# Kernel optimization log

Measured on AMD Instinct MI355X. Metric: run time of the kernel, lower is better.

The kernel has to match this reference:

```python
import jax, jax.numpy as jnp
import numpy as np

ALPHA = 0.2  # LeakyReLU slope
NEG = -1e9


def setup_inputs() -> dict:
    key = jax.random.key(0)
    k1, k2, k3, k4, k5 = jax.random.split(key, 5)
    B, N, F_IN, F_OUT, H = 8, 1024, 512, 256, 8
    x = jax.random.normal(k1, (B, N, F_IN), dtype=jnp.float32)
    adj = jax.random.randint(k2, (B, N, N), 0, 2, dtype=jnp.int32)
    W = jax.random.normal(k3, (H, F_OUT, F_IN), dtype=jnp.float32) * 0.05
    a1 = jax.random.normal(k4, (H, F_OUT), dtype=jnp.float32) * 0.05
    a2 = jax.random.normal(k5, (H, F_OUT), dtype=jnp.float32) * 0.05
    return {"x": x, "adj": adj, "W": W, "a1": a1, "a2": a2}


def _head(x, adj_zero, W, a1, a2):
    # x: (B,N,F_in), W: (F_out,F_in), a1/a2: (F_out,)
    h = jnp.einsum('bnf,of->bno', x, W)              # (B,N,F_out)
    f1 = jnp.einsum('bno,o->bn', h, a1)              # (B,N)
    f2 = jnp.einsum('bno,o->bn', h, a2)              # (B,N)
    e = f1[:, :, None] + f2[:, None, :]              # (B,N,N) broadcast add
    e = jax.nn.leaky_relu(e, negative_slope=ALPHA)
    e = jnp.where(adj_zero, NEG, e)                  # adjacency mask
    att = jax.nn.softmax(e, axis=2)
    return jnp.einsum('bnm,bmo->bno', att, h)        # (B,N,F_out)


def reference(x, adj, W, a1, a2):
    adj_zero = (adj == 0)
    # vmap over heads; sum of elu(head outputs)
    heads = jax.vmap(lambda w, u, v: _head(x, adj_zero, w, u, v))(W, a1, a2)  # (H,B,N,F_out)
    out = jnp.sum(jax.nn.elu(heads), axis=0)         # (B,N,F_out)
    return jax.nn.log_softmax(out, axis=2)
```

## Files before the change

### kernel.cpp

```cpp
#include <hip/hip_runtime.h>
#include <math.h>

#define B_    8
#define N_    1024
#define FIN   512
#define FOUT  256
#define H_    8
#define ALPHA 0.2f

#define XT (B_ * N_ * FIN)
#define WT (H_ * FOUT * FIN)

typedef short s16x8 __attribute__((ext_vector_type(8)));
typedef float f32x4 __attribute__((ext_vector_type(4)));

__device__ __forceinline__ unsigned short f2bf(float f) {
  unsigned int u = __float_as_uint(f);
  u = (u + 0x7FFFu + ((u >> 16) & 1u)) >> 16;
  return (unsigned short)u;
}

__device__ __forceinline__ unsigned int pk4_fp8(float a, float b, float c,
                                                float d) {
  int u = __builtin_amdgcn_cvt_pk_fp8_f32(a, b, 0, false);
  u = __builtin_amdgcn_cvt_pk_fp8_f32(c, d, u, true);
  return (unsigned int)u;
}

#if __has_builtin(__builtin_amdgcn_cvt_pk_f32_fp8)
#define HAVE_DEQ4 1
__device__ __forceinline__ float deq4(unsigned int u) {
  const auto a = __builtin_amdgcn_cvt_pk_f32_fp8((int)u, false);
  const auto b = __builtin_amdgcn_cvt_pk_f32_fp8((int)u, true);
  return (a[0] + a[1]) + (b[0] + b[1]);
}
#else
#define HAVE_DEQ4 0
__device__ __forceinline__ float q8e4m3(float p) {
  if (p >= 0.015625f) {
    unsigned int u = __float_as_uint(p);
    u = (u + 0x7FFFFu + ((u >> 20) & 1u)) & 0xFFF00000u;
    return __uint_as_float(u);
  }
  return (p + 16384.f) - 16384.f;
}
#endif

__device__ __forceinline__ void gload16(const void* g, void* l) {
  __builtin_amdgcn_global_load_lds(
      (const __attribute__((address_space(1))) unsigned int*)g,
      (__attribute__((address_space(3))) unsigned int*)l, 16, 0, 0);
}


#define CVB  ((XT + WT) / 1024)
#define ZRB  192
#define PKB  ((B_ * N_ * 32) / 256)

__global__ __launch_bounds__(256) void prep(
    const float* __restrict__ x, const float* __restrict__ W,
    const int* __restrict__ adj, unsigned short* __restrict__ xb,
    unsigned short* __restrict__ Wb, float* __restrict__ f12,
    unsigned int* __restrict__ adjP) {
  const int blk = blockIdx.x;
  if (blk >= CVB + ZRB) {
    const int dw = (blk - CVB - ZRB) * 256 + threadIdx.x;
    const int r = dw >> 5, pd = dw & 31;
    const int q = pd >> 3, c8 = pd & 7;
    const int* ap = adj + (size_t)r * N_;
    unsigned int out = 0;
#pragma unroll
    for (int i = 0; i < 4; ++i) {
      const int jb = (c8 * 4 + i) * 32 + q * 8;
      int4 v0 = *(const int4*)(ap + jb);
      int4 v1 = *(const int4*)(ap + jb + 4);
      unsigned int byte = 0;
      byte |= (v0.x ? 1u : 0u) << 0; byte |= (v0.y ? 1u : 0u) << 1;
      byte |= (v0.z ? 1u : 0u) << 2; byte |= (v0.w ? 1u : 0u) << 3;
      byte |= (v1.x ? 1u : 0u) << 4; byte |= (v1.y ? 1u : 0u) << 5;
      byte |= (v1.z ? 1u : 0u) << 6; byte |= (v1.w ? 1u : 0u) << 7;
      out |= byte << (i * 8);
    }
    adjP[dw] = out;
    return;
  }
  if (blk >= CVB) {
    const int i = (blk - CVB) * 256 + threadIdx.x;
    ((float4*)f12)[i] = make_float4(0.f, 0.f, 0.f, 0.f);
    return;
  }
  const int i = (blk * 256 + threadIdx.x) * 4;
  const float* src;
  unsigned short* dst;
  int off;
  if (i < XT) { src = x; dst = xb; off = i; }
  else        { src = W; dst = Wb; off = i - XT; }
  float4 v = *(const float4*)(src + off);
  ushort4 s;
  s.x = f2bf(v.x); s.y = f2bf(v.y); s.z = f2bf(v.z); s.w = f2bf(v.w);
  *(ushort4*)(dst + off) = s;
}

__global__ __launch_bounds__(256, 3) void proj_mfma(
    const unsigned short* __restrict__ xb, const unsigned short* __restrict__ Wb,
    const float* __restrict__ a1, const float* __restrict__ a2,
    unsigned char* __restrict__ htq, float* __restrict__ f1,
    float* __restrict__ f2) {
  __shared__ __align__(16) unsigned short As[128 * 64];
  __shared__ __align__(16) unsigned short Bs[128 * 64];
  const int gid = blockIdx.x;
  const int b = gid & 7;
  const int mt_ = (gid >> 3) & 7;
  const int ot_ = (gid >> 6) & 1;
  const int h = gid >> 7;
  const int hb = h * B_ + b;
  const int m0 = mt_ * 128, o0 = ot_ * 128;
  const int t = threadIdx.x, w = t >> 6, lane = t & 63;
  const int col = lane & 15, quad = lane >> 4;

  const int srow = t >> 3;
  const int sseg = (t & 7) ^ (srow & 7);
  const unsigned short* agp = xb + (size_t)(b * N_ + m0 + srow) * FIN + sseg * 8;
  const unsigned short* bgp = Wb + (size_t)(h * FOUT + o0 + srow) * FIN + sseg * 8;

  f32x4 acc[2][8];
  const f32x4 z4 = {0.f, 0.f, 0.f, 0.f};
#pragma unroll
  for (int mt = 0; mt < 2; ++mt)
#pragma unroll
    for (int ot = 0; ot < 8; ++ot) acc[mt][ot] = z4;

  for (int it = 0; it < FIN / 64; ++it) {
    __syncthreads();
    const int k0 = it * 64;
#pragma unroll
    for (int i2 = 0; i2 < 4; ++i2) {
      gload16(agp + (size_t)i2 * 32 * FIN + k0, &As[i2 * 2048 + t * 8]);
      gload16(bgp + (size_t)i2 * 32 * FIN + k0, &Bs[i2 * 2048 + t * 8]);
    }
    __syncthreads();

#pragma unroll
    for (int kb = 0; kb < 2; ++kb) {
      s16x8 af[2], bf[8];
#pragma unroll
      for (int mt = 0; mt < 2; ++mt) {
        const int row = w * 32 + mt * 16 + col;
        af[mt] = *(const s16x8*)&As[row * 64 + ((kb * 4 + quad) ^ (row & 7)) * 8];
      }
#pragma unroll
      for (int ot = 0; ot < 8; ++ot) {
        const int row = ot * 16 + col;
        bf[ot] = *(const s16x8*)&Bs[row * 64 + ((kb * 4 + quad) ^ (row & 7)) * 8];
      }
#pragma unroll
      for (int mt = 0; mt < 2; ++mt)
#pragma unroll
        for (int ot = 0; ot < 8; ++ot)
          acc[mt][ot] = __builtin_amdgcn_mfma_f32_16x16x32_bf16(af[mt], bf[ot],
                                                                acc[mt][ot], 0, 0, 0);
    }
  }

  const int kkw = (m0 >> 5) + w;
  float pf1[2][4] = {{0.f}}, pf2[2][4] = {{0.f}};
#pragma unroll
  for (int mt = 0; mt < 2; ++mt) {
#pragma unroll
    for (int ot = 0; ot < 8; ++ot) {
      const int o = o0 + ot * 16 + col;
      const float va1 = a1[h * FOUT + o], va2 = a2[h * FOUT + o];
      const int otg = (o0 >> 4) + ot;
      unsigned char* fb =
          htq + (((size_t)(hb * 16 + otg) * 32 + kkw) << 9);
      const unsigned int q =
          pk4_fp8(acc[mt][ot][0], acc[mt][ot][1], acc[mt][ot][2], acc[mt][ot][3]);
      *(unsigned int*)(fb + (2 * mt + (quad >> 1)) * 128 + col * 8 +
                       (quad & 1) * 4) = q;
#pragma unroll
      for (int r = 0; r < 4; ++r) {
        pf1[mt][r] += acc[mt][ot][r] * va1;
        pf2[mt][r] += acc[mt][ot][r] * va2;
      }
    }
  }
#pragma unroll
  for (int off = 1; off <= 8; off <<= 1)
#pragma unroll
    for (int mt = 0; mt < 2; ++mt)
#pragma unroll
      for (int r = 0; r < 4; ++r) {
        pf1[mt][r] += __shfl_xor(pf1[mt][r], off);
        pf2[mt][r] += __shfl_xor(pf2[mt][r], off);
      }
  if (col == 0) {
#pragma unroll
    for (int mt = 0; mt < 2; ++mt)
#pragma unroll
      for (int r = 0; r < 4; ++r) {
        const int n = m0 + w * 32 + mt * 16 + quad * 4 + r;
        atomicAdd(&f1[hb * N_ + n], pf1[mt][r]);
        atomicAdd(&f2[hb * N_ + n], pf2[mt][r]);
      }
  }
}

__global__ __launch_bounds__(256) void wgen(
    const float* __restrict__ f1, const float* __restrict__ f2,
    const unsigned int* __restrict__ adjP, unsigned char* __restrict__ wq,
    float* __restrict__ dnm) {
  const int id = blockIdx.x;
  const int b = id & 7, h = (id >> 3) & 7;
  const int rbg = (id >> 6) & 15;
  const int kkh = id >> 10;
  const int w = threadIdx.x >> 6, lane = threadIdx.x & 63;
  const int col = lane & 15, quad = lane >> 4;
  const int hb = h * B_ + b;
  const int rb = rbg * 4 + w;
  const int row = rb * 16 + col;

  const float* f2r = f2 + (size_t)hb * N_;
  float m2 = -3.0e38f;
#pragma unroll
  for (int c = 0; c < 16; ++c) m2 = fmaxf(m2, f2r[lane + c * 64]);
#pragma unroll
  for (int off = 32; off; off >>= 1) m2 = fmaxf(m2, __shfl_xor(m2, off));

  const float f1i = f1[(size_t)hb * N_ + row];
  const float tb = f1i + m2;
  const float mhat = fmaxf(tb, ALPHA * tb);

  const unsigned int* adp = adjP + ((size_t)(b * N_ + row) << 5) + quad * 8;
  const float* f2p = f2r + quad * 8;
  unsigned char* wp = wq + (((size_t)(hb * 64 + rb) * 32) << 9) + lane * 8;

  float dsum = 0.f;
#pragma unroll
  for (int k4i = 0; k4i < 4; ++k4i) {
    const int k4 = kkh * 4 + k4i;
    const unsigned int ad = adp[k4];
#pragma unroll
    for (int k2 = 0; k2 < 4; ++k2) {
      const int kk = k4 * 4 + k2;
      const unsigned int ab = (ad >> (k2 * 8)) & 0xFFu;
      const float4 fA = *(const float4*)(f2p + kk * 32);
      const float4 fB = *(const float4*)(f2p + kk * 32 + 4);
      float ex[8];
#pragma unroll
      for (int j = 0; j < 8; ++j) {
        const float fv = j < 4 ? ((const float*)&fA)[j]
                               : ((const float*)&fB)[j - 4];
        const float tt = f1i + fv;
        const float l = fmaxf(tt, ALPHA * tt);
        const float p = __expf(l - mhat);
        ex[j] = ((ab >> j) & 1u) ? p : 0.f;
      }
      const unsigned int lo = pk4_fp8(ex[0], ex[1], ex[2], ex[3]);
      const unsigned int hi = pk4_fp8(ex[4], ex[5], ex[6], ex[7]);
#if HAVE_DEQ4
      dsum += deq4(lo) + deq4(hi);
#else
#pragma unroll
      for (int j = 0; j < 8; ++j) dsum += q8e4m3(ex[j]);
#endif
      *(uint2*)(wp + kk * 512) = make_uint2(lo, hi);
    }
  }
  dsum += __shfl_xor(dsum, 16);
  dsum += __shfl_xor(dsum, 32);
  if (quad == 0) atomicAdd(&dnm[(size_t)hb * N_ + row], dsum);
}

__global__ __launch_bounds__(256, 4) void pv(
    const unsigned char* __restrict__ htq, const unsigned char* __restrict__ wq,
    const float* __restrict__ dnm, float* __restrict__ p0,
    float* __restrict__ p1, float* __restrict__ p2, float* __restrict__ p3) {
  __shared__ __align__(16) unsigned char Bsh[2][16384];
  const int id = blockIdx.x;
  const int b = id & 7;
  const int g0 = (id >> 3) & 3;
  const int oq = (id >> 5) & 3;
  const int it = id >> 7;
  const int tid = threadIdx.x;
  const int w = tid >> 6, lane = tid & 63;
  const int col = lane & 15, quad = lane >> 4;
  const int rb = it * 8 + w * 2;

  const int hb0 = (g0 * 2 + 0) * B_ + b;
  const int hb1 = (g0 * 2 + 1) * B_ + b;
  const unsigned char* ap0 =
      wq + (((size_t)(hb0 * 64 + rb) * 32) << 9) + lane * 8;
  const unsigned char* ap1 =
      wq + (((size_t)(hb1 * 64 + rb) * 32) << 9) + lane * 8;
  const unsigned char* bp0 = htq + (((size_t)(hb0 * 16 + oq * 4) * 32) << 9);
  const unsigned char* bp1 = htq + (((size_t)(hb1 * 16 + oq * 4) * 32) << 9);

  float hsum[2][4][4];
#pragma unroll
  for (int g = 0; g < 2; ++g)
#pragma unroll
    for (int t = 0; t < 4; ++t)
#pragma unroll
      for (int r = 0; r < 4; ++r) hsum[g][t][r] = 0.f;

  f32x4 acc[2][4];
  const f32x4 z4 = {0.f, 0.f, 0.f, 0.f};
  float4 den0, den1;

#define STAGE(buf, bptr, c)                                                  \
  do {                                                                       \
    _Pragma("unroll")                                                        \
    for (int t = 0; t < 4; ++t)                                              \
      gload16(bptr + t * 16384 + (c) * 4096 + tid * 16,                      \
              &Bsh[buf][t * 4096 + tid * 16]);                               \
  } while (0)

  STAGE(0, bp0, 0);
  __syncthreads();

#pragma unroll
  for (int cc = 0; cc < 8; ++cc) {
    const int hh = cc >> 2;
    const int c = cc & 3;
    const int cur = cc & 1;
    const unsigned char* ap = hh ? ap1 : ap0;

    if (cc < 7) {
      const unsigned char* nbp = ((cc + 1) >> 2) ? bp1 : bp0;
      STAGE(1 - cur, nbp, (cc + 1) & 3);
    }

    if (c == 0) {
      const float* dr = dnm + (size_t)(hh ? hb1 : hb0) * N_ + quad * 4;
      den0 = *(const float4*)(dr + (rb + 0) * 16);
      den1 = *(const float4*)(dr + (rb + 1) * 16);
#pragma unroll
      for (int g = 0; g < 2; ++g)
#pragma unroll
        for (int t = 0; t < 4; ++t) acc[g][t] = z4;
    }

    long A0[8], A1[8];
#pragma unroll
    for (int kkl = 0; kkl < 8; ++kkl) {
      A0[kkl] = *(const long*)(ap + (size_t)(c * 8 + kkl) * 512);
      A1[kkl] = *(const long*)(ap + 16384 + (size_t)(c * 8 + kkl) * 512);
    }

    const unsigned char* bl = &Bsh[cur][lane * 8];
#pragma unroll
    for (int kkl = 0; kkl < 8; ++kkl) {
      const long b0 = *(const long*)(bl + 0 * 4096 + kkl * 512);
      const long b1 = *(const long*)(bl + 1 * 4096 + kkl * 512);
      const long b2 = *(const long*)(bl + 2 * 4096 + kkl * 512);
      const long b3 = *(const long*)(bl + 3 * 4096 + kkl * 512);
      __builtin_amdgcn_s_setprio(1);
      acc[0][0] = __builtin_amdgcn_mfma_f32_16x16x32_fp8_fp8(A0[kkl], b0, acc[0][0], 0, 0, 0);
      acc[1][0] = __builtin_amdgcn_mfma_f32_16x16x32_fp8_fp8(A1[kkl], b0, acc[1][0], 0, 0, 0);
      acc[0][1] = __builtin_amdgcn_mfma_f32_16x16x32_fp8_fp8(A0[kkl], b1, acc[0][1], 0, 0, 0);
      acc[1][1] = __builtin_amdgcn_mfma_f32_16x16x32_fp8_fp8(A1[kkl], b1, acc[1][1], 0, 0, 0);
      acc[0][2] = __builtin_amdgcn_mfma_f32_16x16x32_fp8_fp8(A0[kkl], b2, acc[0][2], 0, 0, 0);
      acc[1][2] = __builtin_amdgcn_mfma_f32_16x16x32_fp8_fp8(A1[kkl], b2, acc[1][2], 0, 0, 0);
      acc[0][3] = __builtin_amdgcn_mfma_f32_16x16x32_fp8_fp8(A0[kkl], b3, acc[0][3], 0, 0, 0);
      acc[1][3] = __builtin_amdgcn_mfma_f32_16x16x32_fp8_fp8(A1[kkl], b3, acc[1][3], 0, 0, 0);
      __builtin_amdgcn_s_setprio(0);
    }

    if (c == 3) {
#pragma unroll
      for (int g = 0; g < 2; ++g)
#pragma unroll
        for (int r = 0; r < 4; ++r) {
          const float dv = (g == 0) ? (&den0.x)[r] : (&den1.x)[r];
          const float inv = 1.0f / dv;
#pragma unroll
          for (int t = 0; t < 4; ++t) {
            const float oh = acc[g][t][r] * inv;
            hsum[g][t][r] += oh > 0.f ? oh : __expf(oh) - 1.f;
          }
        }
    }

    if (cc < 7) __syncthreads();
  }
#undef STAGE

  float* pdst = (g0 == 0) ? p0 : (g0 == 1) ? p1 : (g0 == 2) ? p2 : p3;
#pragma unroll
  for (int g = 0; g < 2; ++g)
#pragma unroll
    for (int t = 0; t < 4; ++t)
#pragma unroll
      for (int r = 0; r < 4; ++r) {
        const int orow = (rb + g) * 16 + quad * 4 + r;
        pdst[(size_t)(b * N_ + orow) * FOUT + oq * 64 + t * 16 + col] =
            hsum[g][t][r];
      }
}

__global__ __launch_bounds__(256) void logsm(
    const float* __restrict__ p0, const float* __restrict__ p1,
    const float* __restrict__ p2, const float* __restrict__ p3,
    float* __restrict__ out) {
  const int row = blockIdx.x * 4 + (threadIdx.x >> 6);
  const int lane = threadIdx.x & 63;
  const size_t base = (size_t)row * FOUT;
  float v[4];
  float m = -3.0e38f;
#pragma unroll
  for (int c = 0; c < 4; ++c) {
    const size_t idx = base + c * 64 + lane;
    v[c] = p0[idx] + p1[idx] + p2[idx] + p3[idx];
    m = fmaxf(m, v[c]);
  }
#pragma unroll
  for (int off = 32; off; off >>= 1) m = fmaxf(m, __shfl_xor(m, off));
  float s = 0.f;
#pragma unroll
  for (int c = 0; c < 4; ++c) s += __expf(v[c] - m);
#pragma unroll
  for (int off = 32; off; off >>= 1) s += __shfl_xor(s, off);
  const float lg = m + logf(s);
#pragma unroll
  for (int c = 0; c < 4; ++c)
    out[base + c * 64 + lane] = v[c] - lg;
}

extern "C" void kernel_launch(void* const* d_in, const int* in_sizes, int n_in,
                              void* d_out, int out_size, void* d_ws,
                              size_t ws_size, hipStream_t stream) {
  const float* x   = (const float*)d_in[0];
  const int*   adj = (const int*)d_in[1];
  const float* W   = (const float*)d_in[2];
  const float* a1  = (const float*)d_in[3];
  const float* a2  = (const float*)d_in[4];
  float* out = (float*)d_out;

  unsigned char* htq = (unsigned char*)d_ws;
  unsigned short* xb = (unsigned short*)(htq + (size_t)H_ * B_ * FOUT * N_);
  unsigned short* Wb = xb + (size_t)XT;
  float* f1 = (float*)(Wb + (size_t)WT);
  float* f2 = f1 + (size_t)H_ * B_ * N_;
  float* dnm = f2 + (size_t)H_ * B_ * N_;
  float* part2 = dnm + (size_t)H_ * B_ * N_;
  float* part3 = part2 + (size_t)B_ * N_ * FOUT;
  unsigned int* adjP = (unsigned int*)(part3 + (size_t)B_ * N_ * FOUT);
  unsigned char* wq = (unsigned char*)(adjP + (size_t)B_ * N_ * 32);
  float* part1 = (float*)xb;

  prep<<<CVB + ZRB + PKB, 256, 0, stream>>>(x, W, adj, xb, Wb, f1, adjP);

  proj_mfma<<<1024, 256, 0, stream>>>(xb, Wb, a1, a2, htq, f1, f2);

  wgen<<<2048, 256, 0, stream>>>(f1, f2, adjP, wq, dnm);

  pv<<<1024, 256, 0, stream>>>(htq, wq, dnm, out, part1, part2, part3);

  logsm<<<(B_ * N_) / 4, 256, 0, stream>>>(out, part1, part2, part3, out);
}
```

Before: 194.6 us.

## Pipeline pv kernel with half-size LDS stages and register-prefetched A operands

Restructures the pv kernel's main loop into 16 smaller phases with half-size double-buffered LDS tiles. The A operands for the next phase are prefetched into ping-pong registers while the current MFMAs run. Barriers now use explicit vmcnt waits instead of __syncthreads, so global loads stay in flight across phases. The launch-bounds occupancy hint is dropped, which gives up the occupancy guarantee in exchange for more registers. The gain is meant to come from hiding global-load latency behind MFMA work, at the cost of more barriers and relying on a hand-tuned vmcnt count.

```diff
diff --git a/kernel.cpp b/kernel.cpp
--- a/kernel.cpp
+++ b/kernel.cpp
@@ -271,11 +271,11 @@
   if (quad == 0) atomicAdd(&dnm[(size_t)hb * N_ + row], dsum);
 }
 
-__global__ __launch_bounds__(256, 4) void pv(
+__global__ __launch_bounds__(256) void pv(
     const unsigned char* __restrict__ htq, const unsigned char* __restrict__ wq,
     const float* __restrict__ dnm, float* __restrict__ p0,
     float* __restrict__ p1, float* __restrict__ p2, float* __restrict__ p3) {
-  __shared__ __align__(16) unsigned char Bsh[2][16384];
+  __shared__ __align__(16) unsigned char Bsh[2][8192];
   const int id = blockIdx.x;
   const int b = id & 7;
   const int g0 = (id >> 3) & 3;
@@ -295,6 +295,10 @@
   const unsigned char* bp0 = htq + (((size_t)(hb0 * 16 + oq * 4) * 32) << 9);
   const unsigned char* bp1 = htq + (((size_t)(hb1 * 16 + oq * 4) * 32) << 9);
 
+  const int flat0 = tid * 16, flat1 = 4096 + tid * 16;
+  const int gs0 = (flat0 >> 11) * 16384 + (flat0 & 2047);
+  const int gs1 = (flat1 >> 11) * 16384 + (flat1 & 2047);
+
   float hsum[2][4][4];
 #pragma unroll
   for (int g = 0; g < 2; ++g)
@@ -306,84 +310,92 @@
   f32x4 acc[2][4];
   const f32x4 z4 = {0.f, 0.f, 0.f, 0.f};
   float4 den0, den1;
-
-#define STAGE(buf, bptr, c)                                                  \
-  do {                                                                       \
-    _Pragma("unroll")                                                        \
-    for (int t = 0; t < 4; ++t)                                              \
-      gload16(bptr + t * 16384 + (c) * 4096 + tid * 16,                      \
-              &Bsh[buf][t * 4096 + tid * 16]);                               \
-  } while (0)
-
-  STAGE(0, bp0, 0);
-  __syncthreads();
-
-#pragma unroll
-  for (int cc = 0; cc < 8; ++cc) {
-    const int hh = cc >> 2;
-    const int c = cc & 3;
-    const int cur = cc & 1;
-    const unsigned char* ap = hh ? ap1 : ap0;
-
-    if (cc < 7) {
-      const unsigned char* nbp = ((cc + 1) >> 2) ? bp1 : bp0;
-      STAGE(1 - cur, nbp, (cc + 1) & 3);
-    }
-
-    if (c == 0) {
-      const float* dr = dnm + (size_t)(hh ? hb1 : hb0) * N_ + quad * 4;
-      den0 = *(const float4*)(dr + (rb + 0) * 16);
-      den1 = *(const float4*)(dr + (rb + 1) * 16);
-#pragma unroll
-      for (int g = 0; g < 2; ++g)
-#pragma unroll
-        for (int t = 0; t < 4; ++t) acc[g][t] = z4;
-    }
-
-    long A0[8], A1[8];
-#pragma unroll
-    for (int kkl = 0; kkl < 8; ++kkl) {
-      A0[kkl] = *(const long*)(ap + (size_t)(c * 8 + kkl) * 512);
-      A1[kkl] = *(const long*)(ap + 16384 + (size_t)(c * 8 + kkl) * 512);
-    }
-
-    const unsigned char* bl = &Bsh[cur][lane * 8];
-#pragma unroll
-    for (int kkl = 0; kkl < 8; ++kkl) {
-      const long b0 = *(const long*)(bl + 0 * 4096 + kkl * 512);
-      const long b1 = *(const long*)(bl + 1 * 4096 + kkl * 512);
-      const long b2 = *(const long*)(bl + 2 * 4096 + kkl * 512);
-      const long b3 = *(const long*)(bl + 3 * 4096 + kkl * 512);
-      __builtin_amdgcn_s_setprio(1);
-      acc[0][0] = __builtin_amdgcn_mfma_f32_16x16x32_fp8_fp8(A0[kkl], b0, acc[0][0], 0, 0, 0);
-      acc[1][0] = __builtin_amdgcn_mfma_f32_16x16x32_fp8_fp8(A1[kkl], b0, acc[1][0], 0, 0, 0);
-      acc[0][1] = __builtin_amdgcn_mfma_f32_16x16x32_fp8_fp8(A0[kkl], b1, acc[0][1], 0, 0, 0);
-      acc[1][1] = __builtin_amdgcn_mfma_f32_16x16x32_fp8_fp8(A1[kkl], b1, acc[1][1], 0, 0, 0);
-      acc[0][2] = __builtin_amdgcn_mfma_f32_16x16x32_fp8_fp8(A0[kkl], b2, acc[0][2], 0, 0, 0);
-      acc[1][2] = __builtin_amdgcn_mfma_f32_16x16x32_fp8_fp8(A1[kkl], b2, acc[1][2], 0, 0, 0);
-      acc[0][3] = __builtin_amdgcn_mfma_f32_16x16x32_fp8_fp8(A0[kkl], b3, acc[0][3], 0, 0, 0);
-      acc[1][3] = __builtin_amdgcn_mfma_f32_16x16x32_fp8_fp8(A1[kkl], b3, acc[1][3], 0, 0, 0);
-      __builtin_amdgcn_s_setprio(0);
-    }
-
-    if (c == 3) {
-#pragma unroll
-      for (int g = 0; g < 2; ++g)
-#pragma unroll
-        for (int r = 0; r < 4; ++r) {
-          const float dv = (g == 0) ? (&den0.x)[r] : (&den1.x)[r];
-          const float inv = 1.0f / dv;
-#pragma unroll
-          for (int t = 0; t < 4; ++t) {
-            const float oh = acc[g][t][r] * inv;
-            hsum[g][t][r] += oh > 0.f ? oh : __expf(oh) - 1.f;
-          }
-        }
-    }
-
-    if (cc < 7) __syncthreads();
-  }
-#undef STAGE
+  long Ae[8], Ao[8];
+
+  {
+    const float* dr = dnm + (size_t)hb0 * N_ + quad * 4;
+    den0 = *(const float4*)(dr + (rb + 0) * 16);
+    den1 = *(const float4*)(dr + (rb + 1) * 16);
+  }
+  gload16(bp0 + gs0, &Bsh[0][flat0]);
+  gload16(bp0 + gs1, &Bsh[0][flat1]);
+#pragma unroll
+  for (int k = 0; k < 4; ++k) {
+    Ae[k] = *(const long*)(ap0 + k * 512);
+    Ae[4 + k] = *(const long*)(ap0 + 16384 + k * 512);
+  }
+  asm volatile("s_waitcnt vmcnt(8)" ::: "memory");
+  __builtin_amdgcn_s_barrier();
+
+#define PHASE(cc, Acur, Anxt)                                                \
+  {                                                                          \
+    const int c_ = (cc) & 7;                                                 \
+    const int cur_ = (cc) & 1;                                               \
+    if ((cc) == 8) {        \
+      const float* dr_ = dnm + (size_t)hb1 * N_ + quad * 4;                  \
+      den0 = *(const float4*)(dr_ + (rb + 0) * 16);                          \
+      den1 = *(const float4*)(dr_ + (rb + 1) * 16);                          \
+    }                                                                        \
+    if ((cc) < 15) {                                                         \
+      const int cn_ = (cc) + 1;                                              \
+      const unsigned char* gb_ = (cn_ >= 8) ? bp1 : bp0;                     \
+      const int co_ = (cn_ & 7) * 2048;                                      \
+      gload16(gb_ + gs0 + co_, &Bsh[1 - cur_][flat0]);                       \
+      gload16(gb_ + gs1 + co_, &Bsh[1 - cur_][flat1]);                       \
+      const unsigned char* an_ = (cn_ >= 8) ? ap1 : ap0;                     \
+      const int ko_ = (cn_ & 7) * 2048;                                      \
+      _Pragma("unroll")                                                      \
+      for (int k = 0; k < 4; ++k) {                                          \
+        Anxt[k] = *(const long*)(an_ + ko_ + k * 512);                       \
+        Anxt[4 + k] = *(const long*)(an_ + 16384 + ko_ + k * 512);           \
+      }                                                                      \
+    }                                                                        \
+    if (c_ == 0) {                                                           \
+      _Pragma("unroll") for (int g = 0; g < 2; ++g)                          \
+      _Pragma("unroll") for (int t = 0; t < 4; ++t) acc[g][t] = z4;          \
+    }                                                                        \
+    {                                                                        \
+      const unsigned char* bl_ = &Bsh[cur_][lane * 8];                       \
+      _Pragma("unroll")                                                      \
+      for (int kkl = 0; kkl < 4; ++kkl) {                                    \
+        const long b0_ = *(const long*)(bl_ + 0 * 2048 + kkl * 512);         \
+        const long b1_ = *(const long*)(bl_ + 1 * 2048 + kkl * 512);         \
+        const long b2_ = *(const long*)(bl_ + 2 * 2048 + kkl * 512);         \
+        const long b3_ = *(const long*)(bl_ + 3 * 2048 + kkl * 512);         \
+        __builtin_amdgcn_s_setprio(1);                                       \
+        acc[0][0] = __builtin_amdgcn_mfma_f32_16x16x32_fp8_fp8(Acur[kkl], b0_, acc[0][0], 0, 0, 0); \
+        acc[1][0] = __builtin_amdgcn_mfma_f32_16x16x32_fp8_fp8(Acur[4 + kkl], b0_, acc[1][0], 0, 0, 0); \
+        acc[0][1] = __builtin_amdgcn_mfma_f32_16x16x32_fp8_fp8(Acur[kkl], b1_, acc[0][1], 0, 0, 0); \
+        acc[1][1] = __builtin_amdgcn_mfma_f32_16x16x32_fp8_fp8(Acur[4 + kkl], b1_, acc[1][1], 0, 0, 0); \
+        acc[0][2] = __builtin_amdgcn_mfma_f32_16x16x32_fp8_fp8(Acur[kkl], b2_, acc[0][2], 0, 0, 0); \
+        acc[1][2] = __builtin_amdgcn_mfma_f32_16x16x32_fp8_fp8(Acur[4 + kkl], b2_, acc[1][2], 0, 0, 0); \
+        acc[0][3] = __builtin_amdgcn_mfma_f32_16x16x32_fp8_fp8(Acur[kkl], b3_, acc[0][3], 0, 0, 0); \
+        acc[1][3] = __builtin_amdgcn_mfma_f32_16x16x32_fp8_fp8(Acur[4 + kkl], b3_, acc[1][3], 0, 0, 0); \
+        __builtin_amdgcn_s_setprio(0);                                       \
+      }                                                                      \
+    }                                                                        \
+    if (c_ == 7) {                \
+      _Pragma("unroll") for (int g = 0; g < 2; ++g)                          \
+      _Pragma("unroll") for (int r = 0; r < 4; ++r) {                        \
+        const float dv_ = (g == 0) ? (&den0.x)[r] : (&den1.x)[r];            \
+        const float inv_ = 1.0f / dv_;                                       \
+        _Pragma("unroll") for (int t = 0; t < 4; ++t) {                      \
+          const float oh_ = acc[g][t][r] * inv_;                             \
+          hsum[g][t][r] += oh_ > 0.f ? oh_ : __expf(oh_) - 1.f;              \
+        }                                                                    \
+      }                                                                      \
+    }                                                                        \
+    if ((cc) < 15) {                                                         \
+      asm volatile("s_waitcnt vmcnt(8)" ::: "memory");       \
+      __builtin_amdgcn_s_barrier();                        \
+    }                                                                        \
+  }
+
+  PHASE(0, Ae, Ao)  PHASE(1, Ao, Ae)  PHASE(2, Ae, Ao)  PHASE(3, Ao, Ae)
+  PHASE(4, Ae, Ao)  PHASE(5, Ao, Ae)  PHASE(6, Ae, Ao)  PHASE(7, Ao, Ae)
+  PHASE(8, Ae, Ao)  PHASE(9, Ao, Ae)  PHASE(10, Ae, Ao) PHASE(11, Ao, Ae)
+  PHASE(12, Ae, Ao) PHASE(13, Ao, Ae) PHASE(14, Ae, Ao) PHASE(15, Ao, Ae)
+#undef PHASE
 
   float* pdst = (g0 == 0) ? p0 : (g0 == 1) ? p1 : (g0 == 2) ? p2 : p3;
 #pragma unroll
```

Result: no change. 191.5 us (median of 2 runs) (-1.6%).

## Fuse attention weight generation into PV kernel, drop wgen and fp8 weight buffer

Applied to the files above, without the earlier changes.

Removes the separate wgen kernel, which wrote fp8 attention weights and denominators to global memory. The pv kernel now computes the exp-weights on the fly from f1, f2 staged in shared memory and the packed adjacency, feeding them straight into the fp8 MFMAs. Work is re-split so each block handles one head and half of the output columns. Per-head ELU outputs go to 8 partial buffers that logsm sums. This avoids a global round trip of the weight tensor and one launch, but recomputes the exps for each output-column half and doubles partial-output traffic. ZRB also drops from 192 to 128 since dnm no longer needs zeroing.

```diff
diff --git a/kernel.cpp b/kernel.cpp
--- a/kernel.cpp
+++ b/kernel.cpp
@@ -52,9 +52,32 @@
       (__attribute__((address_space(3))) unsigned int*)l, 16, 0, 0);
 }
 
+__device__ __forceinline__ long gen8(unsigned int ab, const float4 fA,
+                                     const float4 fB, float f1i, float mhat,
+                                     float& dsum) {
+  float ex[8];
+#pragma unroll
+  for (int j = 0; j < 8; ++j) {
+    const float fv = j < 4 ? ((const float*)&fA)[j] : ((const float*)&fB)[j - 4];
+    const float tt = f1i + fv;
+    const float l = fmaxf(tt, ALPHA * tt);
+    const float p = __expf(l - mhat);
+    ex[j] = ((ab >> j) & 1u) ? p : 0.f;
+  }
+  const unsigned int lo = pk4_fp8(ex[0], ex[1], ex[2], ex[3]);
+  const unsigned int hi = pk4_fp8(ex[4], ex[5], ex[6], ex[7]);
+#if HAVE_DEQ4
+  dsum += deq4(lo) + deq4(hi);
+#else
+#pragma unroll
+  for (int j = 0; j < 8; ++j) dsum += q8e4m3(ex[j]);
+#endif
+  return (long)(((unsigned long long)hi << 32) | (unsigned long long)lo);
+}
+
 
 #define CVB  ((XT + WT) / 1024)
-#define ZRB  192
+#define ZRB  128
 #define PKB  ((B_ * N_ * 32) / 256)
 
 __global__ __launch_bounds__(256) void prep(
@@ -205,212 +228,145 @@
   }
 }
 
-__global__ __launch_bounds__(256) void wgen(
-    const float* __restrict__ f1, const float* __restrict__ f2,
-    const unsigned int* __restrict__ adjP, unsigned char* __restrict__ wq,
-    float* __restrict__ dnm) {
-  const int id = blockIdx.x;
-  const int b = id & 7, h = (id >> 3) & 7;
-  const int rbg = (id >> 6) & 15;
-  const int kkh = id >> 10;
-  const int w = threadIdx.x >> 6, lane = threadIdx.x & 63;
-  const int col = lane & 15, quad = lane >> 4;
-  const int hb = h * B_ + b;
-  const int rb = rbg * 4 + w;
-  const int row = rb * 16 + col;
-
-  const float* f2r = f2 + (size_t)hb * N_;
-  float m2 = -3.0e38f;
-#pragma unroll
-  for (int c = 0; c < 16; ++c) m2 = fmaxf(m2, f2r[lane + c * 64]);
-#pragma unroll
-  for (int off = 32; off; off >>= 1) m2 = fmaxf(m2, __shfl_xor(m2, off));
-
-  const float f1i = f1[(size_t)hb * N_ + row];
-  const float tb = f1i + m2;
-  const float mhat = fmaxf(tb, ALPHA * tb);
-
-  const unsigned int* adp = adjP + ((size_t)(b * N_ + row) << 5) + quad * 8;
-  const float* f2p = f2r + quad * 8;
-  unsigned char* wp = wq + (((size_t)(hb * 64 + rb) * 32) << 9) + lane * 8;
-
-  float dsum = 0.f;
-#pragma unroll
-  for (int k4i = 0; k4i < 4; ++k4i) {
-    const int k4 = kkh * 4 + k4i;
-    const unsigned int ad = adp[k4];
-#pragma unroll
-    for (int k2 = 0; k2 < 4; ++k2) {
-      const int kk = k4 * 4 + k2;
-      const unsigned int ab = (ad >> (k2 * 8)) & 0xFFu;
-      const float4 fA = *(const float4*)(f2p + kk * 32);
-      const float4 fB = *(const float4*)(f2p + kk * 32 + 4);
-      float ex[8];
-#pragma unroll
-      for (int j = 0; j < 8; ++j) {
-        const float fv = j < 4 ? ((const float*)&fA)[j]
-                               : ((const float*)&fB)[j - 4];
-        const float tt = f1i + fv;
-        const float l = fmaxf(tt, ALPHA * tt);
-        const float p = __expf(l - mhat);
-        ex[j] = ((ab >> j) & 1u) ? p : 0.f;
-      }
-      const unsigned int lo = pk4_fp8(ex[0], ex[1], ex[2], ex[3]);
-      const unsigned int hi = pk4_fp8(ex[4], ex[5], ex[6], ex[7]);
-#if HAVE_DEQ4
-      dsum += deq4(lo) + deq4(hi);
-#else
-#pragma unroll
-      for (int j = 0; j < 8; ++j) dsum += q8e4m3(ex[j]);
-#endif
-      *(uint2*)(wp + kk * 512) = make_uint2(lo, hi);
-    }
-  }
-  dsum += __shfl_xor(dsum, 16);
-  dsum += __shfl_xor(dsum, 32);
-  if (quad == 0) atomicAdd(&dnm[(size_t)hb * N_ + row], dsum);
-}
-
 __global__ __launch_bounds__(256, 4) void pv(
-    const unsigned char* __restrict__ htq, const unsigned char* __restrict__ wq,
-    const float* __restrict__ dnm, float* __restrict__ p0,
-    float* __restrict__ p1, float* __restrict__ p2, float* __restrict__ p3) {
+    const unsigned char* __restrict__ htq, const float* __restrict__ f1,
+    const float* __restrict__ f2, const unsigned int* __restrict__ adjP,
+    float* __restrict__ pp) {
   __shared__ __align__(16) unsigned char Bsh[2][16384];
+  __shared__ __align__(16) float f2sh[N_];
   const int id = blockIdx.x;
   const int b = id & 7;
-  const int g0 = (id >> 3) & 3;
-  const int oq = (id >> 5) & 3;
+  const int oc = (id >> 3) & 1;
+  const int h = (id >> 4) & 7;
   const int it = id >> 7;
   const int tid = threadIdx.x;
   const int w = tid >> 6, lane = tid & 63;
   const int col = lane & 15, quad = lane >> 4;
   const int rb = it * 8 + w * 2;
 
-  const int hb0 = (g0 * 2 + 0) * B_ + b;
-  const int hb1 = (g0 * 2 + 1) * B_ + b;
-  const unsigned char* ap0 =
-      wq + (((size_t)(hb0 * 64 + rb) * 32) << 9) + lane * 8;
-  const unsigned char* ap1 =
-      wq + (((size_t)(hb1 * 64 + rb) * 32) << 9) + lane * 8;
-  const unsigned char* bp0 = htq + (((size_t)(hb0 * 16 + oq * 4) * 32) << 9);
-  const unsigned char* bp1 = htq + (((size_t)(hb1 * 16 + oq * 4) * 32) << 9);
-
-  float hsum[2][4][4];
+  const int hb = h * B_ + b;
+  const unsigned char* bp = htq + (((size_t)(hb * 16 + oc * 8) * 32) << 9);
+  const int row0 = rb * 16 + col;
+  const int row1 = row0 + 16;
+  const unsigned int* adp0 = adjP + ((size_t)(b * N_ + row0) << 5) + quad * 8;
+  const unsigned int* adp1 = adjP + ((size_t)(b * N_ + row1) << 5) + quad * 8;
+
+#define STAGE(buf, c)                                                        \
+  {                                                                          \
+    _Pragma("unroll")                                                        \
+    for (int i = 0; i < 4; ++i) {                                            \
+      const int flat = i * 4096 + tid * 16;                                  \
+      gload16(bp + (size_t)(flat >> 11) * 16384 + (c) * 2048 + (flat & 2047),\
+              &Bsh[buf][flat]);                                              \
+    }                                                                        \
+  }
+
+  f32x4 acc[2][8];
+  const f32x4 z4 = {0.f, 0.f, 0.f, 0.f};
 #pragma unroll
   for (int g = 0; g < 2; ++g)
 #pragma unroll
-    for (int t = 0; t < 4; ++t)
-#pragma unroll
-      for (int r = 0; r < 4; ++r) hsum[g][t][r] = 0.f;
-
-  f32x4 acc[2][4];
-  const f32x4 z4 = {0.f, 0.f, 0.f, 0.f};
-  float4 den0, den1;
-
-#define STAGE(buf, bptr, c)                                                  \
-  do {                                                                       \
+    for (int t = 0; t < 8; ++t) acc[g][t] = z4;
+
+  const float* f2r = f2 + (size_t)hb * N_;
+  gload16(f2r + tid * 4, &f2sh[tid * 4]);
+  STAGE(0, 0)
+  float m2 = -3.0e38f;
+#pragma unroll
+  for (int c = 0; c < 16; ++c) m2 = fmaxf(m2, f2r[lane + c * 64]);
+#pragma unroll
+  for (int off = 32; off; off >>= 1) m2 = fmaxf(m2, __shfl_xor(m2, off));
+  const float f1a = f1[(size_t)hb * N_ + row0];
+  const float f1b = f1[(size_t)hb * N_ + row1];
+  const float tb0 = f1a + m2, tb1 = f1b + m2;
+  const float mh0 = fmaxf(tb0, ALPHA * tb0);
+  const float mh1 = fmaxf(tb1, ALPHA * tb1);
+  unsigned int adA0 = adp0[0], adA1 = adp1[0];
+  unsigned int adB0, adB1;
+  float dsum0 = 0.f, dsum1 = 0.f;
+  asm volatile("s_waitcnt vmcnt(0)" ::: "memory");
+  __builtin_amdgcn_s_barrier();
+
+#define PHASE(c, ADC0, ADC1, ADN0, ADN1)                                     \
+  {                                                                          \
+    if ((c) < 7) {                                                           \
+      STAGE(1 - ((c) & 1), (c) + 1)                                          \
+      ADN0 = adp0[(c) + 1];                                                  \
+      ADN1 = adp1[(c) + 1];                                                  \
+    }                                                                        \
     _Pragma("unroll")                                                        \
-    for (int t = 0; t < 4; ++t)                                              \
-      gload16(bptr + t * 16384 + (c) * 4096 + tid * 16,                      \
-              &Bsh[buf][t * 4096 + tid * 16]);                               \
-  } while (0)
-
-  STAGE(0, bp0, 0);
-  __syncthreads();
-
-#pragma unroll
-  for (int cc = 0; cc < 8; ++cc) {
-    const int hh = cc >> 2;
-    const int c = cc & 3;
-    const int cur = cc & 1;
-    const unsigned char* ap = hh ? ap1 : ap0;
-
-    if (cc < 7) {
-      const unsigned char* nbp = ((cc + 1) >> 2) ? bp1 : bp0;
-      STAGE(1 - cur, nbp, (cc + 1) & 3);
+    for (int kkl = 0; kkl < 4; ++kkl) {                                      \
+      const int kk = (c) * 4 + kkl;                                          \
+      const float4 fA = *(const float4*)&f2sh[kk * 32 + quad * 8];           \
+      const float4 fB = *(const float4*)&f2sh[kk * 32 + quad * 8 + 4];       \
+      const long af0 =                                                       \
+          gen8((ADC0 >> (kkl * 8)) & 0xFFu, fA, fB, f1a, mh0, dsum0);        \
+      const long af1 =                                                       \
+          gen8((ADC1 >> (kkl * 8)) & 0xFFu, fA, fB, f1b, mh1, dsum1);        \
+      const unsigned char* bl_ = &Bsh[(c) & 1][kkl * 512 + lane * 8];        \
+      __builtin_amdgcn_s_setprio(1);                                         \
+      _Pragma("unroll")                                                      \
+      for (int t = 0; t < 8; ++t) {                                          \
+        const long bf = *(const long*)(bl_ + t * 2048);                      \
+        acc[0][t] = __builtin_amdgcn_mfma_f32_16x16x32_fp8_fp8(af0, bf, acc[0][t], 0, 0, 0); \
+        acc[1][t] = __builtin_amdgcn_mfma_f32_16x16x32_fp8_fp8(af1, bf, acc[1][t], 0, 0, 0); \
+      }                                                                      \
+      __builtin_amdgcn_s_setprio(0);                                         \
+    }                                                                        \
+    if ((c) < 7) {                                                           \
+      asm volatile("s_waitcnt vmcnt(2)" ::: "memory");    \
+      __builtin_amdgcn_s_barrier();                           \
+    }                                                                        \
+  }
+
+  PHASE(0, adA0, adA1, adB0, adB1)
+  PHASE(1, adB0, adB1, adA0, adA1)
+  PHASE(2, adA0, adA1, adB0, adB1)
+  PHASE(3, adB0, adB1, adA0, adA1)
+  PHASE(4, adA0, adA1, adB0, adB1)
+  PHASE(5, adB0, adB1, adA0, adA1)
+  PHASE(6, adA0, adA1, adB0, adB1)
+  PHASE(7, adB0, adB1, adA0, adA1)
+#undef PHASE
+#undef STAGE
+
+  dsum0 += __shfl_xor(dsum0, 16);
+  dsum0 += __shfl_xor(dsum0, 32);
+  dsum1 += __shfl_xor(dsum1, 16);
+  dsum1 += __shfl_xor(dsum1, 32);
+
+  float* pdst = pp + (size_t)h * ((size_t)B_ * N_ * FOUT);
+#pragma unroll
+  for (int g = 0; g < 2; ++g)
+#pragma unroll
+    for (int r = 0; r < 4; ++r) {
+      const float den = __shfl(g == 0 ? dsum0 : dsum1, quad * 4 + r);
+      const float inv = 1.0f / den;
+      const int orow = (rb + g) * 16 + quad * 4 + r;
+#pragma unroll
+      for (int t = 0; t < 8; ++t) {
+        const float oh = acc[g][t][r] * inv;
+        pdst[(size_t)(b * N_ + orow) * FOUT + oc * 128 + t * 16 + col] =
+            oh > 0.f ? oh : __expf(oh) - 1.f;
+      }
     }
-
-    if (c == 0) {
-      const float* dr = dnm + (size_t)(hh ? hb1 : hb0) * N_ + quad * 4;
-      den0 = *(const float4*)(dr + (rb + 0) * 16);
-      den1 = *(const float4*)(dr + (rb + 1) * 16);
-#pragma unroll
-      for (int g = 0; g < 2; ++g)
-#pragma unroll
-        for (int t = 0; t < 4; ++t) acc[g][t] = z4;
-    }
-
-    long A0[8], A1[8];
-#pragma unroll
-    for (int kkl = 0; kkl < 8; ++kkl) {
-      A0[kkl] = *(const long*)(ap + (size_t)(c * 8 + kkl) * 512);
-      A1[kkl] = *(const long*)(ap + 16384 + (size_t)(c * 8 + kkl) * 512);
-    }
-
-    const unsigned char* bl = &Bsh[cur][lane * 8];
-#pragma unroll
-    for (int kkl = 0; kkl < 8; ++kkl) {
-      const long b0 = *(const long*)(bl + 0 * 4096 + kkl * 512);
-      const long b1 = *(const long*)(bl + 1 * 4096 + kkl * 512);
-      const long b2 = *(const long*)(bl + 2 * 4096 + kkl * 512);
-      const long b3 = *(const long*)(bl + 3 * 4096 + kkl * 512);
-      __builtin_amdgcn_s_setprio(1);
-      acc[0][0] = __builtin_amdgcn_mfma_f32_16x16x32_fp8_fp8(A0[kkl], b0, acc[0][0], 0, 0, 0);
-      acc[1][0] = __builtin_amdgcn_mfma_f32_16x16x32_fp8_fp8(A1[kkl], b0, acc[1][0], 0, 0, 0);
-      acc[0][1] = __builtin_amdgcn_mfma_f32_16x16x32_fp8_fp8(A0[kkl], b1, acc[0][1], 0, 0, 0);
-      acc[1][1] = __builtin_amdgcn_mfma_f32_16x16x32_fp8_fp8(A1[kkl], b1, acc[1][1], 0, 0, 0);
-      acc[0][2] = __builtin_amdgcn_mfma_f32_16x16x32_fp8_fp8(A0[kkl], b2, acc[0][2], 0, 0, 0);
-      acc[1][2] = __builtin_amdgcn_mfma_f32_16x16x32_fp8_fp8(A1[kkl], b2, acc[1][2], 0, 0, 0);
-      acc[0][3] = __builtin_amdgcn_mfma_f32_16x16x32_fp8_fp8(A0[kkl], b3, acc[0][3], 0, 0, 0);
-      acc[1][3] = __builtin_amdgcn_mfma_f32_16x16x32_fp8_fp8(A1[kkl], b3, acc[1][3], 0, 0, 0);
-      __builtin_amdgcn_s_setprio(0);
-    }
-
-    if (c == 3) {
-#pragma unroll
-      for (int g = 0; g < 2; ++g)
-#pragma unroll
-        for (int r = 0; r < 4; ++r) {
-          const float dv = (g == 0) ? (&den0.x)[r] : (&den1.x)[r];
-          const float inv = 1.0f / dv;
-#pragma unroll
-          for (int t = 0; t < 4; ++t) {
-            const float oh = acc[g][t][r] * inv;
-            hsum[g][t][r] += oh > 0.f ? oh : __expf(oh) - 1.f;
-          }
-        }
-    }
-
-    if (cc < 7) __syncthreads();
-  }
-#undef STAGE
-
-  float* pdst = (g0 == 0) ? p0 : (g0 == 1) ? p1 : (g0 == 2) ? p2 : p3;
-#pragma unroll
-  for (int g = 0; g < 2; ++g)
-#pragma unroll
-    for (int t = 0; t < 4; ++t)
-#pragma unroll
-      for (int r = 0; r < 4; ++r) {
-        const int orow = (rb + g) * 16 + quad * 4 + r;
-        pdst[(size_t)(b * N_ + orow) * FOUT + oq * 64 + t * 16 + col] =
-            hsum[g][t][r];
-      }
 }
 
 __global__ __launch_bounds__(256) void logsm(
-    const float* __restrict__ p0, const float* __restrict__ p1,
-    const float* __restrict__ p2, const float* __restrict__ p3,
-    float* __restrict__ out) {
+    const float* __restrict__ pp, float* __restrict__ out) {
   const int row = blockIdx.x * 4 + (threadIdx.x >> 6);
   const int lane = threadIdx.x & 63;
   const size_t base = (size_t)row * FOUT;
+  const size_t PSZ = (size_t)B_ * N_ * FOUT;
   float v[4];
   float m = -3.0e38f;
 #pragma unroll
   for (int c = 0; c < 4; ++c) {
     const size_t idx = base + c * 64 + lane;
-    v[c] = p0[idx] + p1[idx] + p2[idx] + p3[idx];
+    float s = 0.f;
+#pragma unroll
+    for (int hh = 0; hh < 8; ++hh) s += pp[hh * PSZ + idx];
+    v[c] = s;
     m = fmaxf(m, v[c]);
   }
 #pragma unroll
@@ -441,20 +397,17 @@
   unsigned short* Wb = xb + (size_t)XT;
   float* f1 = (float*)(Wb + (size_t)WT);
   float* f2 = f1 + (size_t)H_ * B_ * N_;
-  float* dnm = f2 + (size_t)H_ * B_ * N_;
-  float* part2 = dnm + (size_t)H_ * B_ * N_;
+  float* pad = f2 + (size_t)H_ * B_ * N_;
+  float* part2 = pad + (size_t)H_ * B_ * N_;
   float* part3 = part2 + (size_t)B_ * N_ * FOUT;
   unsigned int* adjP = (unsigned int*)(part3 + (size_t)B_ * N_ * FOUT);
-  unsigned char* wq = (unsigned char*)(adjP + (size_t)B_ * N_ * 32);
-  float* part1 = (float*)xb;
+  float* pp = (float*)(adjP + (size_t)B_ * N_ * 32);
 
   prep<<<CVB + ZRB + PKB, 256, 0, stream>>>(x, W, adj, xb, Wb, f1, adjP);
 
   proj_mfma<<<1024, 256, 0, stream>>>(xb, Wb, a1, a2, htq, f1, f2);
 
-  wgen<<<2048, 256, 0, stream>>>(f1, f2, adjP, wq, dnm);
-
-  pv<<<1024, 256, 0, stream>>>(htq, wq, dnm, out, part1, part2, part3);
-
-  logsm<<<(B_ * N_) / 4, 256, 0, stream>>>(out, part1, part2, part3, out);
-}
+  pv<<<1024, 256, 0, stream>>>(htq, f1, f2, adjP, pp);
+
+  logsm<<<(B_ * N_) / 4, 256, 0, stream>>>(pp, out);
+}
```

Result: slower. 214.5 us (+10.2%).
